# Optimization experiments

Hardware: AMD Instinct MI355X
Metric: run time of the kernel (lower is better)

The kernel has to match this reference:

```python
import jax, jax.numpy as jnp
import numpy as np

NEG_SLOPE = 0.2
EPS = 1e-16


def gatv2_conv(x, src, dst, n_nodes, Wl, Wr, att, bias):
    """GATv2Conv, heads=1, add_self_loops handled by caller via src/dst.
    x: [N, Fin]; src/dst: [E] (message j->i means src=j, dst=i).
    Wl, Wr: [Fin, Fout]; att: [Fout]; bias: [Fout].
    """
    xl = x @ Wl  # [N, Fout] (source transform)
    xr = x @ Wr  # [N, Fout] (target transform)
    # per-edge attention logit: a^T LeakyReLU(xl[j] + xr[i])
    h = xl[src] + xr[dst]                      # [E, Fout]
    e = jax.nn.leaky_relu(h, NEG_SLOPE) @ att  # [E]
    # segment softmax over incoming edges of each dst node
    m = jax.ops.segment_max(e, dst, num_segments=n_nodes)   # [N]
    ex = jnp.exp(e - m[dst])                                 # [E]
    denom = jax.ops.segment_sum(ex, dst, num_segments=n_nodes)  # [N]
    alpha = ex / (denom[dst] + EPS)                          # [E]
    # scatter-aggregate weighted source messages
    out = jax.ops.segment_sum(alpha[:, None] * xl[src], dst, num_segments=n_nodes)
    return out + bias


def glorot(key, shape):
    lim = np.sqrt(6.0 / (shape[0] + shape[1]))
    return jax.random.uniform(key, shape, jnp.float32, -lim, lim)


def setup_inputs() -> dict:
    key = jax.random.key(0)
    ks = jax.random.split(key, 9)
    N, E, Fin, H, Fout = 50000, 800000, 128, 64, 2
    x = jax.random.normal(ks[0], (N, Fin), jnp.float32)
    edge_index = jax.random.randint(ks[1], (2, E), 0, N, jnp.int64)
    return {
        "x": x,
        "edge_index": edge_index,
        "Wl1": glorot(ks[2], (Fin, H)),
        "Wr1": glorot(ks[3], (Fin, H)),
        "att1": glorot(ks[4], (H, 1))[:, 0],
        "b1": jnp.zeros((H,), jnp.float32),
        "Wl2": glorot(ks[5], (H, Fout)),
        "Wr2": glorot(ks[6], (H, Fout)),
        "att2": glorot(ks[7], (Fout, 1))[:, 0],
        "b2": jnp.zeros((Fout,), jnp.float32),
    }


def reference(x, edge_index, Wl1, Wr1, att1, b1, Wl2, Wr2, att2, b2):
    n_nodes = x.shape[0]
    # PyG GATv2Conv adds self-loops by default
    loops = jnp.arange(n_nodes, dtype=edge_index.dtype)
    src = jnp.concatenate([edge_index[0], loops])
    dst = jnp.concatenate([edge_index[1], loops])
    # eval mode: dropout is identity; the initial relu/dropout result is dead code
    h = gatv2_conv(x, src, dst, n_nodes, Wl1, Wr1, att1, b1)
    out = gatv2_conv(h, src, dst, n_nodes, Wl2, Wr2, att2, b2)
    return out
```

## Files before the change

kernel.cpp:

```cpp
#include <hip/hip_runtime.h>
#include <math.h>

#define FIN 128
#define H 64
#define FOUT 2
#define NEG_SLOPE 0.2f
#define EPS 1e-16f

#define SCAN_CHUNK 2048

typedef __attribute__((ext_vector_type(8))) short s8v;
typedef __attribute__((ext_vector_type(4))) float f4v;

__device__ __forceinline__ void load_bs(const int* __restrict__ blocksum, int nscan,
                                        int* bs, int tid){
  if(tid < 64){
    int v = (tid < nscan)? blocksum[tid] : 0;
    int incl = v;
    #pragma unroll
    for(int o=1;o<64;o<<=1){ int u=__shfl_up(incl,o); if(tid>=o) incl+=u; }
    bs[tid] = incl - v;
  }
  __syncthreads();
}

__global__ void k_prep(int* __restrict__ degs, int N4, int ZB,
                       const float* __restrict__ Wl, const float* __restrict__ Wr,
                       unsigned short* __restrict__ pWh, unsigned short* __restrict__ pWe){
  int b = blockIdx.x;
  if(b < ZB){
    int i = b*256 + threadIdx.x;
    if(i < N4) degs[i] = 0;
    return;
  }
  int idx = (b - ZB)*256 + threadIdx.x;
  int lane = idx & 63;
  int ctk  = idx >> 6;
  int k0   = (ctk & 3) * 32;
  int ct   = ctk >> 2;
  int c    = ct*16 + (lane & 15);
  int kb   = k0 + (lane >> 4)*8;
  const float* Wp = (c < 64) ? (Wl + c) : (Wr + (c - 64));
  #pragma unroll
  for(int j=0;j<8;j++){
    float v = Wp[(size_t)(kb + j)*H];
    unsigned u = __float_as_uint(v);
    unsigned short hb = (unsigned short)(u >> 16);
    float hv = __uint_as_float(((unsigned)hb) << 16);
    float ev = v - hv;
    unsigned short eb = (unsigned short)(__float_as_uint(ev) >> 16);
    pWh[(size_t)idx*8 + j] = hb;
    pWe[(size_t)idx*8 + j] = eb;
  }
}

__global__ __launch_bounds__(256) void k_gemm_mfma(
    const float* __restrict__ x,
    const unsigned short* __restrict__ pWh, const unsigned short* __restrict__ pWe,
    float* __restrict__ xr, unsigned short* __restrict__ xlb, int N){
  int tid = threadIdx.x;
  int lane = tid & 63, wid = tid >> 6;
  int rowbase = blockIdx.x*64 + wid*16;
  int r = lane & 15, g = lane >> 4;

  int arow = rowbase + r; if(arow > N-1) arow = N-1;
  const float* xrow = x + (size_t)arow*FIN;
  int orow = rowbase + r;

  s8v xh[4], xe[4];
  #pragma unroll
  for(int k0=0;k0<4;k0++){
    float4 va = *(const float4*)(xrow + k0*32 + g*8);
    float4 vb = *(const float4*)(xrow + k0*32 + g*8 + 4);
    float xs_[8] = {va.x,va.y,va.z,va.w,vb.x,vb.y,vb.z,vb.w};
    #pragma unroll
    for(int j=0;j<8;j++){
      unsigned u = __float_as_uint(xs_[j]);
      unsigned short hb = (unsigned short)(u >> 16);
      xh[k0][j] = (short)hb;
      float ev = xs_[j] - __uint_as_float(((unsigned)hb) << 16);
      xe[k0][j] = (short)(unsigned short)(__float_as_uint(ev) >> 16);
    }
  }

  #pragma unroll 2
  for(int ct=0;ct<8;ct++){
    f4v a = (f4v){0.f,0.f,0.f,0.f};
    #pragma unroll
    for(int k0=0;k0<4;k0++){
      size_t boff = ((size_t)(ct*4 + k0)*64 + lane)*8;
      s8v wh = *(const s8v*)(pWh + boff);
      s8v we = *(const s8v*)(pWe + boff);
      a = __builtin_amdgcn_mfma_f32_16x16x32_bf16(wh, xh[k0], a, 0,0,0);
      a = __builtin_amdgcn_mfma_f32_16x16x32_bf16(wh, xe[k0], a, 0,0,0);
      a = __builtin_amdgcn_mfma_f32_16x16x32_bf16(we, xh[k0], a, 0,0,0);
    }
    if(orow < N){
      if(ct < 4){
        ushort4 pk;
        unsigned u0 = __float_as_uint(a[0]);
        unsigned u1 = __float_as_uint(a[1]);
        unsigned u2 = __float_as_uint(a[2]);
        unsigned u3 = __float_as_uint(a[3]);
        pk.x = (unsigned short)((u0 + 0x7FFF + ((u0>>16)&1)) >> 16);
        pk.y = (unsigned short)((u1 + 0x7FFF + ((u1>>16)&1)) >> 16);
        pk.z = (unsigned short)((u2 + 0x7FFF + ((u2>>16)&1)) >> 16);
        pk.w = (unsigned short)((u3 + 0x7FFF + ((u3>>16)&1)) >> 16);
        *(ushort4*)(xlb + (size_t)orow*H + ct*16 + g*4) = pk;
      } else {
        *(float4*)(xr + (size_t)orow*H + (ct-4)*16 + g*4) =
            make_float4(a[0],a[1],a[2],a[3]);
      }
    }
  }
}

__global__ void k_degree(const int* __restrict__ ei, int E, int Etot, int N,
                         int* __restrict__ degs, int* __restrict__ rank){
  int i0 = (blockIdx.x*blockDim.x + threadIdx.x)*8;
  if(i0 >= Etot) return;
  if(i0 + 8 <= E){
    int4 da = *(const int4*)(ei + E + i0);
    int4 db = *(const int4*)(ei + E + i0 + 4);
    int r0 = atomicAdd(&degs[        da.x],1);
    int r1 = atomicAdd(&degs[        da.y],1);
    int r2 = atomicAdd(&degs[  N +   da.z],1);
    int r3 = atomicAdd(&degs[  N +   da.w],1);
    int r4 = atomicAdd(&degs[2*N +   db.x],1);
    int r5 = atomicAdd(&degs[2*N +   db.y],1);
    int r6 = atomicAdd(&degs[3*N +   db.z],1);
    int r7 = atomicAdd(&degs[3*N +   db.w],1);
    *(int4*)(rank + i0)     = make_int4(r0,r1,r2,r3);
    *(int4*)(rank + i0 + 4) = make_int4(r4,r5,r6,r7);
  } else if(i0 >= E && i0 + 8 <= Etot){
    int v = i0 - E;
    int r0 = atomicAdd(&degs[        v+0],1);
    int r1 = atomicAdd(&degs[        v+1],1);
    int r2 = atomicAdd(&degs[  N +   v+2],1);
    int r3 = atomicAdd(&degs[  N +   v+3],1);
    int r4 = atomicAdd(&degs[2*N +   v+4],1);
    int r5 = atomicAdd(&degs[2*N +   v+5],1);
    int r6 = atomicAdd(&degs[3*N +   v+6],1);
    int r7 = atomicAdd(&degs[3*N +   v+7],1);
    *(int4*)(rank + i0)     = make_int4(r0,r1,r2,r3);
    *(int4*)(rank + i0 + 4) = make_int4(r4,r5,r6,r7);
  } else {
    #pragma unroll
    for(int q=0;q<8;q++){
      int i = i0+q; if(i>=Etot) break;
      int dst = (i<E) ? ei[E+i] : (i-E);
      int s = q >> 1;
      rank[i] = atomicAdd(&degs[s*N + dst],1);
    }
  }
}

__global__ __launch_bounds__(256) void k_scan_a(int* __restrict__ degs, int n,
                                                int* __restrict__ rowptr,
                                                int* __restrict__ blocksum){
  __shared__ int wsum[4];
  int tid = threadIdx.x, lane = tid & 63, wid = tid >> 6;
  int idx = blockIdx.x*SCAN_CHUNK + tid*8;
  int v[8];
  if(idx + 8 <= n){
    int4 a0 = *(const int4*)(degs + idx),         a1 = *(const int4*)(degs + idx + 4);
    int4 b0 = *(const int4*)(degs + n + idx),     b1 = *(const int4*)(degs + n + idx + 4);
    int4 c0 = *(const int4*)(degs + 2*n + idx),   c1 = *(const int4*)(degs + 2*n + idx + 4);
    int4 e0 = *(const int4*)(degs + 3*n + idx),   e1 = *(const int4*)(degs + 3*n + idx + 4);
    *(int4*)(degs + n + idx)     = a0;
    *(int4*)(degs + n + idx + 4) = a1;
    int4 s20 = make_int4(a0.x+b0.x, a0.y+b0.y, a0.z+b0.z, a0.w+b0.w);
    int4 s21 = make_int4(a1.x+b1.x, a1.y+b1.y, a1.z+b1.z, a1.w+b1.w);
    *(int4*)(degs + 2*n + idx)     = s20;
    *(int4*)(degs + 2*n + idx + 4) = s21;
    int4 s30 = make_int4(s20.x+c0.x, s20.y+c0.y, s20.z+c0.z, s20.w+c0.w);
    int4 s31 = make_int4(s21.x+c1.x, s21.y+c1.y, s21.z+c1.z, s21.w+c1.w);
    *(int4*)(degs + 3*n + idx)     = s30;
    *(int4*)(degs + 3*n + idx + 4) = s31;
    v[0]=s30.x+e0.x; v[1]=s30.y+e0.y; v[2]=s30.z+e0.z; v[3]=s30.w+e0.w;
    v[4]=s31.x+e1.x; v[5]=s31.y+e1.y; v[6]=s31.z+e1.z; v[7]=s31.w+e1.w;
  } else {
    #pragma unroll
    for(int i=0;i<8;i++){
      int p = idx+i;
      if(p < n){
        int d0=degs[p], d1=degs[n+p], d2=degs[2*n+p], d3=degs[3*n+p];
        degs[n+p]=d0; degs[2*n+p]=d0+d1; degs[3*n+p]=d0+d1+d2;
        v[i]=d0+d1+d2+d3;
      } else v[i]=0;
    }
  }
  int pre[8]; int st=0;
  #pragma unroll
  for(int i=0;i<8;i++){ pre[i]=st; st+=v[i]; }
  int incl = st;
  #pragma unroll
  for(int o=1;o<64;o<<=1){ int u=__shfl_up(incl,o); if(lane>=o) incl+=u; }
  if(lane==63) wsum[wid]=incl;
  __syncthreads();
  if(tid==0){ int accu=0; for(int i=0;i<4;i++){ int t=wsum[i]; wsum[i]=accu; accu+=t; } }
  __syncthreads();
  int toff = wsum[wid] + incl - st;
  if(idx + 8 <= n){
    int4 o0 = make_int4(toff+pre[0],toff+pre[1],toff+pre[2],toff+pre[3]);
    int4 o1 = make_int4(toff+pre[4],toff+pre[5],toff+pre[6],toff+pre[7]);
    *(int4*)(rowptr+idx)=o0; *(int4*)(rowptr+idx+4)=o1;
  } else {
    #pragma unroll
    for(int i=0;i<8;i++) if(idx+i<n) rowptr[idx+i]=toff+pre[i];
  }
  if(tid==255){
    blocksum[blockIdx.x] = toff + st;
    if(blockIdx.x == gridDim.x-1) rowptr[n] = toff + st;
  }
}

__global__ void k_fill(const int* __restrict__ ei, int E, int Etot, int N,
                       const int* __restrict__ rowptr,
                       const int* __restrict__ blocksum, int nscan,
                       const int* __restrict__ degs,
                       const int* __restrict__ rank, int* __restrict__ csr_src){
  __shared__ int bs[64];
  int tid = threadIdx.x;
  load_bs(blocksum, nscan, bs, tid);
  int i0 = (blockIdx.x*blockDim.x + tid)*8;
  if(i0 >= Etot) return;
  if(i0 + 8 <= E){
    int4 sa = *(const int4*)(ei + i0);
    int4 sb = *(const int4*)(ei + i0 + 4);
    int4 da = *(const int4*)(ei + E + i0);
    int4 db = *(const int4*)(ei + E + i0 + 4);
    int4 ra = *(const int4*)(rank + i0);
    int4 rb = *(const int4*)(rank + i0 + 4);
    csr_src[rowptr[da.x] + bs[da.x>>11] +                   ra.x] = sa.x;
    csr_src[rowptr[da.y] + bs[da.y>>11] +                   ra.y] = sa.y;
    csr_src[rowptr[da.z] + bs[da.z>>11] + degs[  N + da.z] + ra.z] = sa.z;
    csr_src[rowptr[da.w] + bs[da.w>>11] + degs[  N + da.w] + ra.w] = sa.w;
    csr_src[rowptr[db.x] + bs[db.x>>11] + degs[2*N + db.x] + rb.x] = sb.x;
    csr_src[rowptr[db.y] + bs[db.y>>11] + degs[2*N + db.y] + rb.y] = sb.y;
    csr_src[rowptr[db.z] + bs[db.z>>11] + degs[3*N + db.z] + rb.z] = sb.z;
    csr_src[rowptr[db.w] + bs[db.w>>11] + degs[3*N + db.w] + rb.w] = sb.w;
  } else if(i0 >= E && i0 + 8 <= Etot){
    int4 ra = *(const int4*)(rank + i0);
    int4 rb = *(const int4*)(rank + i0 + 4);
    int v = i0 - E;
    csr_src[rowptr[v+0] + bs[(v+0)>>11] +                    ra.x] = v+0;
    csr_src[rowptr[v+1] + bs[(v+1)>>11] +                    ra.y] = v+1;
    csr_src[rowptr[v+2] + bs[(v+2)>>11] + degs[  N + (v+2)] + ra.z] = v+2;
    csr_src[rowptr[v+3] + bs[(v+3)>>11] + degs[  N + (v+3)] + ra.w] = v+3;
    csr_src[rowptr[v+4] + bs[(v+4)>>11] + degs[2*N + (v+4)] + rb.x] = v+4;
    csr_src[rowptr[v+5] + bs[(v+5)>>11] + degs[2*N + (v+5)] + rb.y] = v+5;
    csr_src[rowptr[v+6] + bs[(v+6)>>11] + degs[3*N + (v+6)] + rb.z] = v+6;
    csr_src[rowptr[v+7] + bs[(v+7)>>11] + degs[3*N + (v+7)] + rb.w] = v+7;
  } else {
    #pragma unroll
    for(int q=0;q<8;q++){
      int i = i0+q; if(i>=Etot) break;
      int src, dst;
      if(i<E){ src = ei[i]; dst = ei[E+i]; } else { src = i-E; dst = i-E; }
      int s = q >> 1;
      int so = s ? degs[s*N + dst] : 0;
      csr_src[rowptr[dst] + bs[dst>>11] + so + rank[i]] = src;
    }
  }
}

__global__ void k_node1f(const int* __restrict__ rowptr, const int* __restrict__ blocksum,
                         int nscan, const int* __restrict__ csr_src,
                         const unsigned short* __restrict__ xlb, const float* __restrict__ xr,
                         const float* __restrict__ att, const float* __restrict__ b1,
                         const float* __restrict__ Wl2, const float* __restrict__ Wr2,
                         float* __restrict__ xl2, float* __restrict__ xr2, int N){
  __shared__ int bs[64];
  int tid = threadIdx.x;
  load_bs(blocksum, nscan, bs, tid);
  int node = blockIdx.x*16 + (tid>>4);
  int gl = tid & 15;
  if(node >= N) return;
  int f4 = gl*4;
  float4 attv = *(const float4*)(att + f4);
  float4 xrv  = *(const float4*)(xr + (size_t)node*H + f4);
  int s = rowptr[node]   + bs[node>>11];
  int t = rowptr[node+1] + bs[(node+1)>>11];
  float d = 0.f;
  float ax=0.f, ay=0.f, az=0.f, aw=0.f;

  for(int k=s; k<t; k+=8){
    int tl = t - 1;
    int ks[8]; float4 xv[8]; float msk[8];
    #pragma unroll
    for(int j=0;j<8;j++){
      int kj = k + j;
      ks[j] = (kj < t) ? kj : tl;
      msk[j] = (kj < t) ? 1.f : 0.f;
    }
    int ss[8];
    #pragma unroll
    for(int j=0;j<8;j++) ss[j] = csr_src[ks[j]];
    #pragma unroll
    for(int j=0;j<8;j++){
      ushort4 uv = *(const ushort4*)(xlb + (size_t)ss[j]*H + f4);
      xv[j].x = __uint_as_float((unsigned)uv.x << 16);
      xv[j].y = __uint_as_float((unsigned)uv.y << 16);
      xv[j].z = __uint_as_float((unsigned)uv.z << 16);
      xv[j].w = __uint_as_float((unsigned)uv.w << 16);
    }
    #pragma unroll
    for(int j=0;j<8;j++){
      float h0 = xv[j].x + xrv.x, h1 = xv[j].y + xrv.y;
      float h2 = xv[j].z + xrv.z, h3 = xv[j].w + xrv.w;
      float l0 = (h0>0.f)? h0 : NEG_SLOPE*h0;
      float l1 = (h1>0.f)? h1 : NEG_SLOPE*h1;
      float l2 = (h2>0.f)? h2 : NEG_SLOPE*h2;
      float l3 = (h3>0.f)? h3 : NEG_SLOPE*h3;
      float e = l0*attv.x + l1*attv.y + l2*attv.z + l3*attv.w;
      #pragma unroll
      for(int o=1;o<16;o<<=1) e += __shfl_xor(e,o);
      float w = msk[j] * __expf(e);
      d  += w;
      ax += w*xv[j].x; ay += w*xv[j].y; az += w*xv[j].z; aw += w*xv[j].w;
    }
  }

  float inv = 1.f/(d + EPS);
  float4 bv = *(const float4*)(b1 + f4);
  float h0 = ax*inv + bv.x, h1 = ay*inv + bv.y;
  float h2 = az*inv + bv.z, h3 = aw*inv + bv.w;
  float p0 = h0*Wl2[(f4+0)*FOUT+0] + h1*Wl2[(f4+1)*FOUT+0] + h2*Wl2[(f4+2)*FOUT+0] + h3*Wl2[(f4+3)*FOUT+0];
  float p1 = h0*Wl2[(f4+0)*FOUT+1] + h1*Wl2[(f4+1)*FOUT+1] + h2*Wl2[(f4+2)*FOUT+1] + h3*Wl2[(f4+3)*FOUT+1];
  float p2 = h0*Wr2[(f4+0)*FOUT+0] + h1*Wr2[(f4+1)*FOUT+0] + h2*Wr2[(f4+2)*FOUT+0] + h3*Wr2[(f4+3)*FOUT+0];
  float p3 = h0*Wr2[(f4+0)*FOUT+1] + h1*Wr2[(f4+1)*FOUT+1] + h2*Wr2[(f4+2)*FOUT+1] + h3*Wr2[(f4+3)*FOUT+1];
  #pragma unroll
  for(int o=1;o<16;o<<=1){
    p0 += __shfl_xor(p0,o); p1 += __shfl_xor(p1,o);
    p2 += __shfl_xor(p2,o); p3 += __shfl_xor(p3,o);
  }
  if(gl==0){
    *(float2*)(xl2 + node*2) = make_float2(p0,p1);
    *(float2*)(xr2 + node*2) = make_float2(p2,p3);
  }
}

__global__ void k_node2(const int* __restrict__ rowptr, const int* __restrict__ blocksum,
                        int nscan, const int* __restrict__ csr_src,
                        const float* __restrict__ xl2, const float* __restrict__ xr2,
                        const float* __restrict__ att2, const float* __restrict__ b2,
                        float* __restrict__ out, int N){
  __shared__ int bs[64];
  int tid = threadIdx.x;
  load_bs(blocksum, nscan, bs, tid);
  int node = blockIdx.x*16 + (tid>>4);
  int gl = tid & 15;
  if(node >= N) return;
  int s = rowptr[node]   + bs[node>>11];
  int t = rowptr[node+1] + bs[(node+1)>>11];
  float2 xrv = *(const float2*)(xr2 + node*2);
  float a0 = att2[0], a1 = att2[1];
  float den=0.f, n0=0.f, n1=0.f;
  for(int k=s+gl; k<t; k+=16){
    int src = csr_src[k];
    float2 xs = *(const float2*)(xl2 + src*2);
    float h0 = xs.x + xrv.x, h1 = xs.y + xrv.y;
    float l0 = (h0>0.f)? h0 : NEG_SLOPE*h0;
    float l1 = (h1>0.f)? h1 : NEG_SLOPE*h1;
    float ex = __expf(l0*a0 + l1*a1);
    den += ex; n0 += ex*xs.x; n1 += ex*xs.y;
  }
  #pragma unroll
  for(int o=1;o<16;o<<=1){
    den += __shfl_xor(den,o);
    n0  += __shfl_xor(n0,o);
    n1  += __shfl_xor(n1,o);
  }
  if(gl==0){
    float inv = 1.f/(den + EPS);
    out[node*2+0] = n0*inv + b2[0];
    out[node*2+1] = n1*inv + b2[1];
  }
}

extern "C" void kernel_launch(void* const* d_in, const int* in_sizes, int n_in,
                              void* d_out, int out_size, void* d_ws, size_t ws_size,
                              hipStream_t stream){
  const float* x    = (const float*)d_in[0];
  const int*   ei   = (const int*)d_in[1];
  const float* Wl1  = (const float*)d_in[2];
  const float* Wr1  = (const float*)d_in[3];
  const float* att1 = (const float*)d_in[4];
  const float* b1   = (const float*)d_in[5];
  const float* Wl2  = (const float*)d_in[6];
  const float* Wr2  = (const float*)d_in[7];
  const float* att2 = (const float*)d_in[8];
  const float* b2   = (const float*)d_in[9];
  int N = in_sizes[0]/FIN;
  int E = in_sizes[1]/2;
  int Etot = E + N;
  int nscan = (N + SCAN_CHUNK - 1) / SCAN_CHUNK;
  int noct  = (Etot + 7) / 8;
  int ZB = (4*N + 255) / 256;
  int GDO = (noct + 255) / 256;

  char* w = (char*)d_ws;
  size_t off = 0;
  auto alloc = [&](size_t bytes)->void*{
    void* p = w + off;
    off = (off + bytes + 255) & ~(size_t)255;
    return p;
  };
  float* xr1     = (float*)alloc((size_t)N*H*4);
  unsigned short* xlb = (unsigned short*)alloc((size_t)N*H*2);
  int*   csr_src = (int*)  alloc((size_t)Etot*4);
  int*   rank    = (int*)  alloc((size_t)Etot*4);
  int*   degs    = (int*)  alloc((size_t)4*N*4);
  int*   rowptr  = (int*)  alloc((size_t)(N+1)*4);
  int*   blocksum= (int*)  alloc((size_t)64*4);
  float* xl2     = (float*)alloc((size_t)N*2*4);
  float* xr2     = (float*)alloc((size_t)N*2*4);
  unsigned short* pWh = (unsigned short*)alloc((size_t)2048*8*2);
  unsigned short* pWe = (unsigned short*)alloc((size_t)2048*8*2);

  k_prep<<<ZB+8, 256, 0, stream>>>(degs, 4*N, ZB, Wl1, Wr1, pWh, pWe);
  k_gemm_mfma<<<(N+63)/64, 256, 0, stream>>>(x, pWh, pWe, xr1, xlb, N);
  k_degree<<<GDO,256,0,stream>>>(ei, E, Etot, N, degs, rank);
  k_scan_a<<<nscan,256,0,stream>>>(degs, N, rowptr, blocksum);
  k_fill<<<GDO,256,0,stream>>>(ei, E, Etot, N, rowptr, blocksum, nscan, degs, rank, csr_src);
  k_node1f<<<(N+15)/16, 256, 0, stream>>>(rowptr, blocksum, nscan, csr_src,
                                          xlb, xr1, att1, b1, Wl2, Wr2, xl2, xr2, N);
  k_node2<<<(N+15)/16, 256, 0, stream>>>(rowptr, blocksum, nscan, csr_src,
                                         xl2, xr2, att2, b2, (float*)d_out, N);
}
```

Baseline: 122.9 us.

## Reorder nodes by in-degree via histogram counting sort for load balance

Builds a 256-bin histogram of node in-degrees during the scan, prefix-sums the bins, and computes a degree-sorted permutation of nodes. The node aggregation kernels then process nodes in perm order so that the 16-lane groups within a wavefront handle nodes of similar degree, reducing divergence in the edge loop. This adds two small kernel launches plus an extra indirection per node, and xr/output accesses are no longer contiguous across groups.

```diff
diff --git a/kernel.cpp b/kernel.cpp
--- a/kernel.cpp
+++ b/kernel.cpp
@@ -24,13 +24,13 @@
   __syncthreads();
 }
 
-__global__ void k_prep(int* __restrict__ degs, int N4, int ZB,
+__global__ void k_prep(int* __restrict__ degs, int NZ, int ZB,
                        const float* __restrict__ Wl, const float* __restrict__ Wr,
                        unsigned short* __restrict__ pWh, unsigned short* __restrict__ pWe){
   int b = blockIdx.x;
   if(b < ZB){
     int i = b*256 + threadIdx.x;
-    if(i < N4) degs[i] = 0;
+    if(i < NZ) degs[i] = 0;
     return;
   }
   int idx = (b - ZB)*256 + threadIdx.x;
@@ -157,9 +157,12 @@
 
 __global__ __launch_bounds__(256) void k_scan_a(int* __restrict__ degs, int n,
                                                 int* __restrict__ rowptr,
-                                                int* __restrict__ blocksum){
+                                                int* __restrict__ blocksum,
+                                                int* __restrict__ hist){
   __shared__ int wsum[4];
+  __shared__ int lh[256];
   int tid = threadIdx.x, lane = tid & 63, wid = tid >> 6;
+  lh[tid] = 0;
   int idx = blockIdx.x*SCAN_CHUNK + tid*8;
   int v[8];
   if(idx + 8 <= n){
@@ -190,6 +193,11 @@
       } else v[i]=0;
     }
   }
+  __syncthreads();
+  #pragma unroll
+  for(int i=0;i<8;i++){
+    if(idx+i < n) atomicAdd(&lh[min(v[i],255)], 1);
+  }
   int pre[8]; int st=0;
   #pragma unroll
   for(int i=0;i<8;i++){ pre[i]=st; st+=v[i]; }
@@ -209,10 +217,48 @@
     #pragma unroll
     for(int i=0;i<8;i++) if(idx+i<n) rowptr[idx+i]=toff+pre[i];
   }
+  if(lh[tid] > 0) atomicAdd(&hist[tid], lh[tid]);
   if(tid==255){
     blocksum[blockIdx.x] = toff + st;
     if(blockIdx.x == gridDim.x-1) rowptr[n] = toff + st;
   }
+}
+
+__global__ void k_binscan(const int* __restrict__ hist, int* __restrict__ bincur){
+  __shared__ int ws4[4];
+  int tid = threadIdx.x, lane = tid & 63, wid = tid >> 6;
+  int v = hist[tid];
+  int incl = v;
+  #pragma unroll
+  for(int o=1;o<64;o<<=1){ int u=__shfl_up(incl,o); if(lane>=o) incl+=u; }
+  if(lane==63) ws4[wid]=incl;
+  __syncthreads();
+  if(tid==0){ int acc=0; for(int i=0;i<4;i++){ int t=ws4[i]; ws4[i]=acc; acc+=t; } }
+  __syncthreads();
+  bincur[tid*16] = ws4[wid] + incl - v;
+}
+
+__global__ __launch_bounds__(256) void k_perm(const int* __restrict__ rowptr,
+                                              const int* __restrict__ blocksum, int nscan,
+                                              int* __restrict__ bincur,
+                                              int* __restrict__ perm, int N){
+  __shared__ int bs[64];
+  __shared__ int lh[256];
+  __shared__ int gbase[256];
+  int tid = threadIdx.x;
+  lh[tid] = 0;
+  load_bs(blocksum, nscan, bs, tid);
+  int slot = blockIdx.x*256 + tid;
+  int b = 0, lrank = 0;
+  if(slot < N){
+    int deg = (rowptr[slot+1] + bs[(slot+1)>>11]) - (rowptr[slot] + bs[slot>>11]);
+    b = min(deg, 255);
+    lrank = atomicAdd(&lh[b], 1);
+  }
+  __syncthreads();
+  if(lh[tid] > 0) gbase[tid] = atomicAdd(&bincur[tid*16], lh[tid]);
+  __syncthreads();
+  if(slot < N) perm[gbase[b] + lrank] = slot;
 }
 
 __global__ void k_fill(const int* __restrict__ ei, int E, int Etot, int N,
@@ -267,6 +313,7 @@
 
 __global__ void k_node1f(const int* __restrict__ rowptr, const int* __restrict__ blocksum,
                          int nscan, const int* __restrict__ csr_src,
+                         const int* __restrict__ perm,
                          const unsigned short* __restrict__ xlb, const float* __restrict__ xr,
                          const float* __restrict__ att, const float* __restrict__ b1,
                          const float* __restrict__ Wl2, const float* __restrict__ Wr2,
@@ -274,9 +321,10 @@
   __shared__ int bs[64];
   int tid = threadIdx.x;
   load_bs(blocksum, nscan, bs, tid);
-  int node = blockIdx.x*16 + (tid>>4);
+  int slot = blockIdx.x*16 + (tid>>4);
   int gl = tid & 15;
-  if(node >= N) return;
+  if(slot >= N) return;
+  int node = perm[slot];
   int f4 = gl*4;
   float4 attv = *(const float4*)(att + f4);
   float4 xrv  = *(const float4*)(xr + (size_t)node*H + f4);
@@ -343,15 +391,17 @@
 
 __global__ void k_node2(const int* __restrict__ rowptr, const int* __restrict__ blocksum,
                         int nscan, const int* __restrict__ csr_src,
+                        const int* __restrict__ perm,
                         const float* __restrict__ xl2, const float* __restrict__ xr2,
                         const float* __restrict__ att2, const float* __restrict__ b2,
                         float* __restrict__ out, int N){
   __shared__ int bs[64];
   int tid = threadIdx.x;
   load_bs(blocksum, nscan, bs, tid);
-  int node = blockIdx.x*16 + (tid>>4);
+  int slot = blockIdx.x*16 + (tid>>4);
   int gl = tid & 15;
-  if(node >= N) return;
+  if(slot >= N) return;
+  int node = perm[slot];
   int s = rowptr[node]   + bs[node>>11];
   int t = rowptr[node+1] + bs[(node+1)>>11];
   float2 xrv = *(const float2*)(xr2 + node*2);
@@ -397,7 +447,6 @@
   int Etot = E + N;
   int nscan = (N + SCAN_CHUNK - 1) / SCAN_CHUNK;
   int noct  = (Etot + 7) / 8;
-  int ZB = (4*N + 255) / 256;
   int GDO = (noct + 255) / 256;
 
   char* w = (char*)d_ws;
@@ -412,6 +461,9 @@
   int*   csr_src = (int*)  alloc((size_t)Etot*4);
   int*   rank    = (int*)  alloc((size_t)Etot*4);
   int*   degs    = (int*)  alloc((size_t)4*N*4);
+  int*   hist    = (int*)  alloc((size_t)256*4);
+  int*   bincur  = (int*)  alloc((size_t)256*16*4);
+  int*   perm    = (int*)  alloc((size_t)N*4);
   int*   rowptr  = (int*)  alloc((size_t)(N+1)*4);
   int*   blocksum= (int*)  alloc((size_t)64*4);
   float* xl2     = (float*)alloc((size_t)N*2*4);
@@ -419,13 +471,18 @@
   unsigned short* pWh = (unsigned short*)alloc((size_t)2048*8*2);
   unsigned short* pWe = (unsigned short*)alloc((size_t)2048*8*2);
 
-  k_prep<<<ZB+8, 256, 0, stream>>>(degs, 4*N, ZB, Wl1, Wr1, pWh, pWe);
+  int NZ = 4*N + 256;
+  int ZB = (NZ + 255) / 256;
+
+  k_prep<<<ZB+8, 256, 0, stream>>>(degs, NZ, ZB, Wl1, Wr1, pWh, pWe);
   k_gemm_mfma<<<(N+63)/64, 256, 0, stream>>>(x, pWh, pWe, xr1, xlb, N);
   k_degree<<<GDO,256,0,stream>>>(ei, E, Etot, N, degs, rank);
-  k_scan_a<<<nscan,256,0,stream>>>(degs, N, rowptr, blocksum);
+  k_scan_a<<<nscan,256,0,stream>>>(degs, N, rowptr, blocksum, hist);
+  k_binscan<<<1,256,0,stream>>>(hist, bincur);
+  k_perm<<<(N+255)/256,256,0,stream>>>(rowptr, blocksum, nscan, bincur, perm, N);
   k_fill<<<GDO,256,0,stream>>>(ei, E, Etot, N, rowptr, blocksum, nscan, degs, rank, csr_src);
-  k_node1f<<<(N+15)/16, 256, 0, stream>>>(rowptr, blocksum, nscan, csr_src,
+  k_node1f<<<(N+15)/16, 256, 0, stream>>>(rowptr, blocksum, nscan, csr_src, perm,
                                           xlb, xr1, att1, b1, Wl2, Wr2, xl2, xr2, N);
-  k_node2<<<(N+15)/16, 256, 0, stream>>>(rowptr, blocksum, nscan, csr_src,
+  k_node2<<<(N+15)/16, 256, 0, stream>>>(rowptr, blocksum, nscan, csr_src, perm,
                                          xl2, xr2, att2, b2, (float*)d_out, N);
 }
```

After: 131.3 us. +6.8%, slower.
